# Optimization experiments

Hardware: AMD Instinct MI355X
Metric: run time of the kernel (lower is better)

The kernel has to match this reference:

```python
import jax, jax.numpy as jnp
import numpy as np

B, T, D, H = 4, 2048, 1024, 16
HD = D // H


def setup_inputs() -> dict:
    key = jax.random.key(0)
    ks = jax.random.split(key, 10)
    s = 1.0 / np.sqrt(D)
    # xavier_uniform bound for wbias [T,T]: sqrt(6/(T+T))
    wb_bound = float(np.sqrt(6.0 / (T + T)))
    return {
        "x": jax.random.normal(ks[0], (B, T, D), dtype=jnp.float32),
        "Wq": jax.random.normal(ks[1], (D, D), dtype=jnp.float32) * s,
        "bq": jnp.zeros((D,), dtype=jnp.float32),
        "Wk": jax.random.normal(ks[2], (D, D), dtype=jnp.float32) * s,
        "bk": jnp.zeros((D,), dtype=jnp.float32),
        "Wv": jax.random.normal(ks[3], (D, D), dtype=jnp.float32) * s,
        "bv": jnp.zeros((D,), dtype=jnp.float32),
        "Wo": jax.random.normal(ks[4], (D, D), dtype=jnp.float32) * s,
        "bo": jnp.zeros((D,), dtype=jnp.float32),
        "wbias": jax.random.uniform(ks[5], (T, T), dtype=jnp.float32,
                                    minval=-wb_bound, maxval=wb_bound),
    }


def reference(x, Wq, bq, Wk, bk, Wv, bv, Wo, bo, wbias):
    Bc, Tc, Dc = x.shape
    # projections, split heads: [B, H, T, HD]
    def proj(W, b):
        y = x @ W + b
        return y.reshape(Bc, Tc, H, HD).transpose(0, 2, 1, 3)

    Q = proj(Wq, bq)
    K = proj(Wk, bk)
    V = proj(Wv, bv)

    Q_sig = jax.nn.sigmoid(Q)
    eK = jnp.exp(K)                      # [B,H,T,HD]
    ew = jnp.exp(wbias[:Tc, :Tc])        # [T,T]

    num = jnp.einsum('ts,bhsd->bhtd', ew, eK * V)
    den = jnp.einsum('ts,bhsd->bhtd', ew, eK)
    out = Q_sig * (num / den)            # [B,H,T,HD]

    out = out.transpose(0, 2, 1, 3).reshape(Bc, Tc, Dc)
    return out @ Wo + bo
```

## Files before the change

kernel.cpp:

```cpp
#include <hip/hip_runtime.h>
#include <hip/hip_bf16.h>


#define AS1(p) ((const __attribute__((address_space(1))) void*)(p))
#define AS3(p) ((__attribute__((address_space(3))) void*)(p))

typedef _Float16 half8 __attribute__((ext_vector_type(8)));
typedef _Float16 half4v __attribute__((ext_vector_type(4)));
typedef float floatx16 __attribute__((ext_vector_type(16)));
typedef int intx4 __attribute__((ext_vector_type(4)));
typedef int intx8 __attribute__((ext_vector_type(8)));

__device__ __forceinline__ long frag_off(int r, int k) {
  return (long)(((((r >> 5) * 4 + (k >> 4)) * 2 + ((k >> 3) & 1)) * 32 + (r & 31)) * 8 + (k & 7));
}
__device__ __forceinline__ long off8(int r, int k) {
  return (long)((((((r >> 5) * 2 + ((k >> 6) & 1)) * 2 + ((k >> 4) & 1)) * 2 + ((k >> 5) & 1)) * 32 +
                 (r & 31)) * 16 + (k & 15));
}

__global__ __launch_bounds__(256) void prep_all(
    const float* __restrict__ x, const float* __restrict__ wb, const float* __restrict__ Wq,
    const float* __restrict__ Wk, const float* __restrict__ Wv, const float* __restrict__ Wo,
    _Float16* __restrict__ x_h, char* __restrict__ E8, _Float16* __restrict__ WqkvT,
    _Float16* __restrict__ WoT, float* __restrict__ cs) {
  __shared__ _Float16 lds[64 * 132];
  const int bid = blockIdx.x;
  const int tid = threadIdx.x;

  if (bid >= 1792) {
    float4 z = {0.f, 0.f, 0.f, 0.f};
#pragma unroll
    for (int p = 0; p < 8; ++p) *(float4*)(cs + (p * 256 + tid) * 4) = z;
    return;
  }

  if (bid < 1024) {
    const int tm = bid >> 4, tk = bid & 15;
    const long tbase = (long)bid * 8192;
#pragma unroll
    for (int p = 0; p < 4; ++p) {
      const int s = p * 256 + tid;
      const int r = ((s >> 8) << 5) + (s & 31);
      const int k = ((s >> 6) & 3) * 16 + ((s >> 5) & 1) * 8;
      const float* sp = x + (long)(tm * 128 + r) * 1024 + tk * 64 + k;
      const float4 v0 = *(const float4*)sp;
      const float4 v1 = *(const float4*)(sp + 4);
      half8 h;
      h[0] = (_Float16)v0.x; h[1] = (_Float16)v0.y; h[2] = (_Float16)v0.z; h[3] = (_Float16)v0.w;
      h[4] = (_Float16)v1.x; h[5] = (_Float16)v1.y; h[6] = (_Float16)v1.z; h[7] = (_Float16)v1.w;
      *(half8*)(x_h + tbase + (long)s * 8) = h;
    }
    return;
  }

  if (bid >= 1536) {
    const int e = bid - 1536;
    const int tt = e >> 4, ts = e & 15;
    char* dst = E8 + (long)e * 16384;
#pragma unroll
    for (int p = 0; p < 16; ++p) {
      const int idx = p * 256 + tid;
      const int r = idx >> 5, k = (idx & 31) * 4;
      const float4 v = *(const float4*)(wb + (long)(tt * 128 + r) * 2048 + ts * 128 + k);
      const float e0 = (__expf(v.x) - 1.0f) * 32.0f, e1 = (__expf(v.y) - 1.0f) * 32.0f;
      const float e2 = (__expf(v.z) - 1.0f) * 32.0f, e3 = (__expf(v.w) - 1.0f) * 32.0f;
      int pk = __builtin_amdgcn_cvt_pk_fp8_f32(e0, e1, 0, false);
      pk = __builtin_amdgcn_cvt_pk_fp8_f32(e2, e3, pk, true);
      *(int*)(dst + off8(r, k)) = pk;
    }
    return;
  }

  const int b2 = bid - 1024;
  const float* src0;
  const float* src1 = nullptr;
  _Float16* dst;
  int tn, tk, cb = 0;
  if (b2 < 128) {
    tn = b2 >> 4; tk = b2 & 15; src0 = Wq; dst = WqkvT;
  } else if (b2 < 384) {
    const int t = b2 - 128;
    tn = 8 + (t >> 4); tk = t & 15; cb = (tn - 8) * 64; src0 = Wk; src1 = Wv; dst = WqkvT;
  } else {
    const int t = b2 - 384;
    tn = t >> 4; tk = t & 15; src0 = Wo; dst = WoT;
  }
  if (!src1) {
#pragma unroll
    for (int p = 0; p < 8; ++p) {
      const int kl = p * 8 + (tid >> 5);
      const int cl = (tid & 31) * 4;
      const float4 v = *(const float4*)(src0 + (long)(tk * 64 + kl) * 1024 + tn * 128 + cl);
      half4v h;
      h[0] = (_Float16)v.x; h[1] = (_Float16)v.y; h[2] = (_Float16)v.z; h[3] = (_Float16)v.w;
      *(half4v*)(lds + kl * 132 + cl) = h;
    }
  } else {
#pragma unroll
    for (int m = 0; m < 2; ++m) {
      const float* s = m ? src1 : src0;
      const int rb = m ? 32 : 0;
#pragma unroll
      for (int p = 0; p < 4; ++p) {
        const int kl = p * 16 + (tid >> 4);
        const int cl = (tid & 15) * 4;
        const int rl = (cl >> 5) * 64 + rb + (cl & 31);
        const float4 v = *(const float4*)(s + (long)(tk * 64 + kl) * 1024 + cb + cl);
        half4v h;
        h[0] = (_Float16)v.x; h[1] = (_Float16)v.y; h[2] = (_Float16)v.z; h[3] = (_Float16)v.w;
        *(half4v*)(lds + kl * 132 + rl) = h;
      }
    }
  }
  __syncthreads();
  const long tbase = (long)(tn * 16 + tk) * 8192;
#pragma unroll
  for (int p = 0; p < 4; ++p) {
    const int s = p * 256 + tid;
    const int r = ((s >> 8) << 5) + (s & 31);
    const int kl = ((s >> 6) & 3) * 16 + ((s >> 5) & 1) * 8;
    half8 h;
#pragma unroll
    for (int j = 0; j < 8; ++j) h[j] = lds[(kl + j) * 132 + r];
    *(half8*)(dst + tbase + (long)s * 8) = h;
  }
}

template <int KS>
__device__ __forceinline__ void rd_ab(const _Float16* sA, const _Float16* sB, int wm, int wn,
                                      int lane, half8 (&a)[2], half8 (&b)[2]) {
  a[0] = *(const half8*)(sA + (((wm >> 5) + 0) * 4 + KS) * 512 + lane * 8);
  a[1] = *(const half8*)(sA + (((wm >> 5) + 1) * 4 + KS) * 512 + lane * 8);
  b[0] = *(const half8*)(sB + (((wn >> 5) + 0) * 4 + KS) * 512 + lane * 8);
  b[1] = *(const half8*)(sB + (((wn >> 5) + 1) * 4 + KS) * 512 + lane * 8);
}

__device__ __forceinline__ void mm4(const half8 (&a)[2], const half8 (&b)[2],
                                    floatx16 (&acc)[2][2]) {
  __builtin_amdgcn_s_setprio(1);
#pragma unroll
  for (int mt = 0; mt < 2; ++mt)
#pragma unroll
    for (int nt = 0; nt < 2; ++nt)
      acc[mt][nt] = __builtin_amdgcn_mfma_f32_32x32x16_f16(a[mt], b[nt], acc[mt][nt], 0, 0, 0);
  __builtin_amdgcn_s_setprio(0);
}

template <int VM, bool STAGE, bool LAST>
__device__ __forceinline__ void tile_step(int t, const _Float16* __restrict__ Ablk,
                                          const _Float16* __restrict__ Bblk, _Float16* ring,
                                          int tid, int lane, int wm, int wn,
                                          half8 (&a0)[2], half8 (&b0)[2], half8 (&a1)[2],
                                          half8 (&b1)[2], floatx16 (&acc)[2][2]) {
  const _Float16* sA = ring + (t % 3) * 8192;
  const _Float16* sB = ring + 24576 + (t % 3) * 16384;
  if (STAGE) {
    const int ts = t + 2;
    _Float16* dA = ring + (ts % 3) * 8192 + tid * 8;
    _Float16* dB = ring + 24576 + (ts % 3) * 16384 + tid * 8;
    const _Float16* gA = Ablk + (long)ts * 8192 + tid * 8;
    const _Float16* gB = Bblk + (long)ts * 8192 + tid * 8;
    __builtin_amdgcn_global_load_lds(AS1(gA), AS3(dA), 16, 0, 0);
    __builtin_amdgcn_global_load_lds(AS1(gA + 4096), AS3(dA + 4096), 16, 0, 0);
    __builtin_amdgcn_global_load_lds(AS1(gB), AS3(dB), 16, 0, 0);
    __builtin_amdgcn_global_load_lds(AS1(gB + 4096), AS3(dB + 4096), 16, 0, 0);
    __builtin_amdgcn_global_load_lds(AS1(gB + 131072), AS3(dB + 8192), 16, 0, 0);
    __builtin_amdgcn_global_load_lds(AS1(gB + 131072 + 4096), AS3(dB + 12288), 16, 0, 0);
  }
  rd_ab<1>(sA, sB, wm, wn, lane, a1, b1);
  mm4(a0, b0, acc);
  rd_ab<2>(sA, sB, wm, wn, lane, a0, b0);
  mm4(a1, b1, acc);
  rd_ab<3>(sA, sB, wm, wn, lane, a1, b1);
  mm4(a0, b0, acc);
  if (!LAST) {
    asm volatile("s_waitcnt vmcnt(%0)" ::"i"(VM < 0 ? 0 : VM) : "memory");
    __builtin_amdgcn_s_barrier();
    asm volatile("" ::: "memory");
    const _Float16* nA = ring + ((t + 1) % 3) * 8192;
    const _Float16* nB = ring + 24576 + ((t + 1) % 3) * 16384;
    rd_ab<0>(nA, nB, wm, wn, lane, a0, b0);
  }
  mm4(a1, b1, acc);
}

template <int MODE>
__global__ __launch_bounds__(512, 1) void gemm_bt2(
    const _Float16* __restrict__ A, const _Float16* __restrict__ Bt, void* __restrict__ Cv,
    const float* __restrict__ bias0, const float* __restrict__ bias1,
    const float* __restrict__ bias2, char* __restrict__ Zt8, float* __restrict__ cs) {
  __shared__ __align__(16) _Float16 ring[73728];
  const int tid = threadIdx.x;
  const int wid = tid >> 6, lane = tid & 63;
  const int l32 = lane & 31, khalf = lane >> 5;

  const int f = blockIdx.x;
  const int j = f >> 3;
  const int bxs = (f & 7) * 8 + (j & 7);
  const int bys = j >> 3;
  const int m0 = bxs * 128, n0 = bys * 256;
  const int wm = (wid >> 2) * 64, wn = (wid & 3) * 64;

  const _Float16* Ablk = A + (long)bxs * 131072;
  const _Float16* Bblk = Bt + (long)(bys * 2) * 131072;

#pragma unroll
  for (int t0 = 0; t0 < 2; ++t0) {
    _Float16* dA = ring + t0 * 8192 + tid * 8;
    _Float16* dB = ring + 24576 + t0 * 16384 + tid * 8;
    const _Float16* gA = Ablk + (long)t0 * 8192 + tid * 8;
    const _Float16* gB = Bblk + (long)t0 * 8192 + tid * 8;
    __builtin_amdgcn_global_load_lds(AS1(gA), AS3(dA), 16, 0, 0);
    __builtin_amdgcn_global_load_lds(AS1(gA + 4096), AS3(dA + 4096), 16, 0, 0);
    __builtin_amdgcn_global_load_lds(AS1(gB), AS3(dB), 16, 0, 0);
    __builtin_amdgcn_global_load_lds(AS1(gB + 4096), AS3(dB + 4096), 16, 0, 0);
    __builtin_amdgcn_global_load_lds(AS1(gB + 131072), AS3(dB + 8192), 16, 0, 0);
    __builtin_amdgcn_global_load_lds(AS1(gB + 131072 + 4096), AS3(dB + 12288), 16, 0, 0);
  }
  asm volatile("s_waitcnt vmcnt(6)" ::: "memory");
  __builtin_amdgcn_s_barrier();
  asm volatile("" ::: "memory");

  half8 a0[2], b0[2], a1[2], b1[2];
  rd_ab<0>(ring, ring + 24576, wm, wn, lane, a0, b0);

  floatx16 acc[2][2] = {};
#pragma unroll
  for (int t = 0; t < 14; ++t)
    tile_step<6, true, false>(t, Ablk, Bblk, ring, tid, lane, wm, wn, a0, b0, a1, b1, acc);
  tile_step<0, false, false>(14, Ablk, Bblk, ring, tid, lane, wm, wn, a0, b0, a1, b1, acc);
  tile_step<0, false, true>(15, Ablk, Bblk, ring, tid, lane, wm, wn, a0, b0, a1, b1, acc);

  if (MODE == 0) {
    if (n0 < 1024) {
      _Float16* Qs = (_Float16*)Cv;
#pragma unroll
      for (int mt = 0; mt < 2; ++mt) {
        const long ttile = (m0 + wm + mt * 32) >> 5;
#pragma unroll
        for (int nt = 0; nt < 2; ++nt) {
          const int col = n0 + wn + nt * 32 + l32;
          const float bb = bias0[col];
          const long base = (ttile * 32 + (((n0 + wn) >> 5) + nt)) * 1024;
#pragma unroll
          for (int q = 0; q < 4; ++q) {
            half4v o;
#pragma unroll
            for (int rr = 0; rr < 4; ++rr) {
              const float v = acc[mt][nt][q * 4 + rr] + bb;
              o[rr] = (_Float16)(1.0f / (1.0f + __expf(-v)));
            }
            *(half4v*)(Qs + base + q * 256 + lane * 4) = o;
          }
        }
      }
    } else {
      const int grp = (n0 - 1024 + wn) >> 6;
      const int ch = grp * 32 + l32;
      const float bkc = bias1[ch], bvc = bias2[ch];
      const int jn = grp * 64 + l32;
      const int b = m0 >> 11;
      char* Z8 = Zt8 + (long)b * 4194304 +
                 ((long)(jn >> 7) * 16 + ((m0 & 2047) >> 7)) * 16384;
      const int jnl = jn & 127;
      float sk = 0.f, sz = 0.f;
#pragma unroll
      for (int mt = 0; mt < 2; ++mt) {
#pragma unroll
        for (int q = 0; q < 4; ++q) {
          float ekv[4], ekk[4];
#pragma unroll
          for (int rr = 0; rr < 4; ++rr) {
            const float ek = __expf(acc[mt][0][q * 4 + rr] + bkc);
            const float vv = acc[mt][1][q * 4 + rr] + bvc;
            ekk[rr] = ek;
            ekv[rr] = ek * vv;
            sk += ek;
            sz += ek * vv;
          }
          const int sl = wm + mt * 32 + 4 * khalf + 8 * q;
          int pn = __builtin_amdgcn_cvt_pk_fp8_f32(ekv[0] * 0.25f, ekv[1] * 0.25f, 0, false);
          pn = __builtin_amdgcn_cvt_pk_fp8_f32(ekv[2] * 0.25f, ekv[3] * 0.25f, pn, true);
          int pd = __builtin_amdgcn_cvt_pk_fp8_f32(ekk[0] * 0.25f, ekk[1] * 0.25f, 0, false);
          pd = __builtin_amdgcn_cvt_pk_fp8_f32(ekk[2] * 0.25f, ekk[3] * 0.25f, pd, true);
          *(int*)(Z8 + off8(jnl, sl)) = pn;
          *(int*)(Z8 + off8(jnl + 32, sl)) = pd;
        }
      }
      atomicAdd(&cs[(long)b * 2048 + ch * 2], sz);
      atomicAdd(&cs[(long)b * 2048 + ch * 2 + 1], sk);
    }
    return;
  }

#pragma unroll
  for (int mt = 0; mt < 2; ++mt)
#pragma unroll
    for (int nt = 0; nt < 2; ++nt) {
      const int col = n0 + wn + nt * 32 + l32;
      const float bb = bias0[col];
#pragma unroll
      for (int reg = 0; reg < 16; ++reg) {
        const int row = m0 + wm + mt * 32 + 4 * khalf + 8 * (reg >> 2) + (reg & 3);
        ((float*)Cv)[(long)row * 1024 + col] = acc[mt][nt][reg] + bb;
      }
    }
}

template <int VM, bool STAGE, int SLOT>
__device__ __forceinline__ void g2_phase(int g, char* __restrict__ ringA, char* __restrict__ ringB,
                                         const char* At0, const char* At1,
                                         const char* Bt0, const char* Bt1,
                                         int tid, int lane, int wm, int wn,
                                         floatx16 (&acc)[2][4]) {
  const int l32 = lane & 31, khalf = lane >> 5;
  intx8 a8[2], b8[4];
  {
    const int G = (wm >> 5);
    const char* pa = ringA + SLOT * 16384 + (G >> 2) * 8192 + (G & 3) * 2048 + khalf * 512 + l32 * 16;
    const intx4 alo = *(const intx4*)pa;
    const intx4 ahi = *(const intx4*)(pa + 1024);
    a8[0] = __builtin_shufflevector(alo, ahi, 0, 1, 2, 3, 4, 5, 6, 7);
  }
#pragma unroll
  for (int nt = 0; nt < 2; ++nt) {
    const int Gn = (wn >> 5) + nt;
    const char* pb = ringB + SLOT * 16384 + (Gn >> 2) * 8192 + (Gn & 3) * 2048 + khalf * 512 + l32 * 16;
    const intx4 blo = *(const intx4*)pb;
    const intx4 bhi = *(const intx4*)(pb + 1024);
    b8[nt] = __builtin_shufflevector(blo, bhi, 0, 1, 2, 3, 4, 5, 6, 7);
  }
  {
    const int G = (wm >> 5) + 1;
    const char* pa = ringA + SLOT * 16384 + (G >> 2) * 8192 + (G & 3) * 2048 + khalf * 512 + l32 * 16;
    const intx4 alo = *(const intx4*)pa;
    const intx4 ahi = *(const intx4*)(pa + 1024);
    a8[1] = __builtin_shufflevector(alo, ahi, 0, 1, 2, 3, 4, 5, 6, 7);
  }
#pragma unroll
  for (int nt = 2; nt < 4; ++nt) {
    const int Gn = (wn >> 5) + nt;
    const char* pb = ringB + SLOT * 16384 + (Gn >> 2) * 8192 + (Gn & 3) * 2048 + khalf * 512 + l32 * 16;
    const intx4 blo = *(const intx4*)pb;
    const intx4 bhi = *(const intx4*)(pb + 1024);
    b8[nt] = __builtin_shufflevector(blo, bhi, 0, 1, 2, 3, 4, 5, 6, 7);
  }
  if (STAGE) {
    const int ks = g + 2;
    constexpr int SS = (SLOT + 2) % 3;
    const long gsrc = (long)(ks >> 1) * 16384 + (long)(tid >> 7) * 4096 + (long)(ks & 1) * 2048 +
                      (tid & 127) * 16;
    char* dA = ringA + SS * 16384 + tid * 16;
    char* dB = ringB + SS * 16384 + tid * 16;
    __builtin_amdgcn_global_load_lds(AS1(At0 + gsrc), AS3(dA), 16, 0, 0);
    __builtin_amdgcn_global_load_lds(AS1(At1 + gsrc), AS3(dA + 8192), 16, 0, 0);
    __builtin_amdgcn_global_load_lds(AS1(Bt0 + gsrc), AS3(dB), 16, 0, 0);
    __builtin_amdgcn_global_load_lds(AS1(Bt1 + gsrc), AS3(dB + 8192), 16, 0, 0);
  }
  if constexpr (VM >= 0) {
    asm volatile("s_waitcnt vmcnt(%0)" ::"i"(VM) : "memory");
    __builtin_amdgcn_s_barrier();
  }
  __builtin_amdgcn_s_setprio(1);
#pragma unroll
  for (int nt = 0; nt < 4; ++nt)
#pragma unroll
    for (int mt = 0; mt < 2; ++mt)
      acc[mt][nt] = __builtin_amdgcn_mfma_scale_f32_32x32x64_f8f6f4(
          a8[mt], b8[nt], acc[mt][nt], 0, 0, 0, 127u, 0, 127u);
  __builtin_amdgcn_s_setprio(0);
  if constexpr (VM >= 0) {
    __builtin_amdgcn_s_barrier();
    asm volatile("" ::: "memory");
  }
}

__global__ __launch_bounds__(512, 1) void gemm2_fp8(
    const char* __restrict__ E8, const char* __restrict__ Zt8, _Float16* __restrict__ OH,
    const _Float16* __restrict__ Qsig, const float* __restrict__ cs) {
  __shared__ __align__(16) char ring[98304];
  char* ringA = ring;
  char* ringB = ring + 49152;
  const int tid = threadIdx.x;
  const int wid = tid >> 6, lane = tid & 63;
  const int l32 = lane & 31, khalf = lane >> 5;

  const int f = blockIdx.x;
  const int bxs = f & 7;
  const int bys = (f >> 3) & 7;
  const int bzs = f >> 6;
  const int m0 = bxs * 256;
  const int wm = (wid >> 1) * 64, wn = (wid & 1) * 128;

  const char* At0 = E8 + (long)(bxs * 2) * 262144;
  const char* At1 = At0 + 262144;
  const char* Bt0 = Zt8 + (long)bzs * 4194304 + (long)(bys * 2) * 262144;
  const char* Bt1 = Bt0 + 262144;

#pragma unroll
  for (int ks = 0; ks < 2; ++ks) {
    const long gsrc = (long)(tid >> 7) * 4096 + (long)(ks & 1) * 2048 + (tid & 127) * 16;
    char* dA = ringA + ks * 16384 + tid * 16;
    char* dB = ringB + ks * 16384 + tid * 16;
    __builtin_amdgcn_global_load_lds(AS1(At0 + gsrc), AS3(dA), 16, 0, 0);
    __builtin_amdgcn_global_load_lds(AS1(At1 + gsrc), AS3(dA + 8192), 16, 0, 0);
    __builtin_amdgcn_global_load_lds(AS1(Bt0 + gsrc), AS3(dB), 16, 0, 0);
    __builtin_amdgcn_global_load_lds(AS1(Bt1 + gsrc), AS3(dB + 8192), 16, 0, 0);
  }
  asm volatile("s_waitcnt vmcnt(4)" ::: "memory");
  __builtin_amdgcn_s_barrier();
  asm volatile("" ::: "memory");

  floatx16 acc[2][4] = {};
#pragma unroll 1
  for (int gb = 0; gb < 30; gb += 3) {
    g2_phase<4, true, 0>(gb + 0, ringA, ringB, At0, At1, Bt0, Bt1, tid, lane, wm, wn, acc);
    g2_phase<4, true, 1>(gb + 1, ringA, ringB, At0, At1, Bt0, Bt1, tid, lane, wm, wn, acc);
    g2_phase<4, true, 2>(gb + 2, ringA, ringB, At0, At1, Bt0, Bt1, tid, lane, wm, wn, acc);
  }
  g2_phase<0, false, 0>(30, ringA, ringB, At0, At1, Bt0, Bt1, tid, lane, wm, wn, acc);
  g2_phase<-1, false, 1>(31, ringA, ringB, At0, At1, Bt0, Bt1, tid, lane, wm, wn, acc);

  const int g32b = bys * 4 + (wn >> 6);
#pragma unroll
  for (int mt = 0; mt < 2; ++mt) {
    const long ttile = (long)(bzs * 2048 + m0 + wm + mt * 32) >> 5;
#pragma unroll
    for (int p = 0; p < 2; ++p) {
      const int g32 = g32b + p;
      const int ch = g32 * 32 + l32;
      const float2 c2 = *(const float2*)(cs + (long)bzs * 2048 + ch * 2);
      const long qbase = (ttile * 32 + g32) * 1024;
#pragma unroll
      for (int q = 0; q < 4; ++q) {
        const half4v qv = *(const half4v*)(Qsig + qbase + q * 256 + lane * 4);
#pragma unroll
        for (int rr = 0; rr < 4; ++rr) {
          const int reg = q * 4 + rr;
          const float num = c2.x + acc[mt][2 * p][reg] * 0.125f;
          const float den = c2.y + acc[mt][2 * p + 1][reg] * 0.125f;
          const int r = m0 + wm + mt * 32 + 4 * khalf + 8 * q + rr;
          const int R = bzs * 2048 + r;
          const long off = ((long)(R >> 7) * 16 + (ch >> 6)) * 8192 + frag_off(R & 127, ch & 63);
          OH[off] = (_Float16)((float)qv[rr] * num / den);
        }
      }
    }
  }
}

extern "C" void kernel_launch(void* const* d_in, const int* in_sizes, int n_in, void* d_out,
                              int out_size, void* d_ws, size_t ws_size, hipStream_t stream) {
  const float* x = (const float*)d_in[0];
  const float* Wq = (const float*)d_in[1];
  const float* bq = (const float*)d_in[2];
  const float* Wk = (const float*)d_in[3];
  const float* bk = (const float*)d_in[4];
  const float* Wv = (const float*)d_in[5];
  const float* bv = (const float*)d_in[6];
  const float* Wo = (const float*)d_in[7];
  const float* bo = (const float*)d_in[8];
  const float* wb = (const float*)d_in[9];

  char* ws = (char*)d_ws;
  _Float16* x_h = (_Float16*)(ws + 0);
  _Float16* WqkvT = (_Float16*)(ws + 16777216);
  _Float16* WoT = (_Float16*)(ws + 23068672);
  char* E8 = (char*)(ws + 25165824);
  _Float16* Qsig = (_Float16*)(ws + 29360128);
  char* Zt8 = (char*)(ws + 46137344);
  _Float16* OutHead = (_Float16*)(ws + 62914560);
  float* cs = (float*)(ws + 79691776);

  prep_all<<<1793, 256, 0, stream>>>(x, wb, Wq, Wk, Wv, Wo, x_h, E8, WqkvT, WoT, cs);

  gemm_bt2<0><<<768, 512, 0, stream>>>(x_h, WqkvT, Qsig, bq, bk, bv, Zt8, cs);

  gemm2_fp8<<<256, 512, 0, stream>>>(E8, Zt8, OutHead, Qsig, cs);

  gemm_bt2<2><<<256, 512, 0, stream>>>(OutHead, WoT, d_out, bo, nullptr, nullptr, nullptr, nullptr);
}
```

Baseline: 245.9 us.

## Enlarge GEMM tiles to 256x256 with split-phase A/B staging pipeline

Replaces the 128x256 projection GEMM with a 256x256 tile per block, where each wave computes a 128x64 output using four row fragments. A keeps a three-slot ring, while B keeps a single buffer refilled in K-halves between barriers. Loads are interleaved across four MFMA phases per K-step. This raises arithmetic intensity and halves the block count. The cost is more barriers per step, more accumulator registers, and fewer blocks (384 and 128), which may underfill the 256 CUs.

```diff
diff --git a/kernel.cpp b/kernel.cpp
--- a/kernel.cpp
+++ b/kernel.cpp
@@ -10,6 +10,10 @@
 typedef float floatx16 __attribute__((ext_vector_type(16)));
 typedef int intx4 __attribute__((ext_vector_type(4)));
 typedef int intx8 __attribute__((ext_vector_type(8)));
+
+__device__ __forceinline__ floatx16 MM(half8 a, half8 b, floatx16 c) {
+  return __builtin_amdgcn_mfma_f32_32x32x16_f16(a, b, c, 0, 0, 0);
+}
 
 __device__ __forceinline__ long frag_off(int r, int k) {
   return (long)(((((r >> 5) * 4 + (k >> 4)) * 2 + ((k >> 3) & 1)) * 32 + (r & 31)) * 8 + (k & 7));
@@ -127,128 +131,182 @@
   }
 }
 
-template <int KS>
-__device__ __forceinline__ void rd_ab(const _Float16* sA, const _Float16* sB, int wm, int wn,
-                                      int lane, half8 (&a)[2], half8 (&b)[2]) {
-  a[0] = *(const half8*)(sA + (((wm >> 5) + 0) * 4 + KS) * 512 + lane * 8);
-  a[1] = *(const half8*)(sA + (((wm >> 5) + 1) * 4 + KS) * 512 + lane * 8);
-  b[0] = *(const half8*)(sB + (((wn >> 5) + 0) * 4 + KS) * 512 + lane * 8);
-  b[1] = *(const half8*)(sB + (((wn >> 5) + 1) * 4 + KS) * 512 + lane * 8);
-}
-
-__device__ __forceinline__ void mm4(const half8 (&a)[2], const half8 (&b)[2],
-                                    floatx16 (&acc)[2][2]) {
+template <bool SA, bool SB, int VM2>
+__device__ __forceinline__ void step3(
+    int t, const _Float16* __restrict__ As0, const _Float16* __restrict__ As1,
+    const _Float16* __restrict__ Bb, _Float16* ldsA, _Float16* ldsB,
+    int tid, int lane, int wmh, const _Float16* bb, floatx16 (&acc)[4][2]) {
+  const _Float16* sA = ldsA + (t % 3) * 16384 + wmh * 8192 + lane * 8;
+  half8 a[4], b[4];
+
+  asm volatile("s_waitcnt vmcnt(2)" ::: "memory");
+  __builtin_amdgcn_s_barrier();
+  asm volatile("" ::: "memory");
+  a[0] = *(const half8*)(sA + 0 * 512);
+  a[1] = *(const half8*)(sA + 1 * 512);
+  a[2] = *(const half8*)(sA + 4 * 512);
+  a[3] = *(const half8*)(sA + 5 * 512);
+  b[0] = *(const half8*)(bb + 0);
+  b[1] = *(const half8*)(bb + 512);
+  b[2] = *(const half8*)(bb + 1024);
+  b[3] = *(const half8*)(bb + 1536);
+  if (SA) {
+    _Float16* d = ldsA + ((t + 2) % 3) * 16384 + tid * 8;
+    const _Float16* g = As0 + (long)(t + 2) * 8192 + tid * 8;
+    __builtin_amdgcn_global_load_lds(AS1(g), AS3(d), 16, 0, 0);
+    __builtin_amdgcn_global_load_lds(AS1(g + 4096), AS3(d + 4096), 16, 0, 0);
+  }
   __builtin_amdgcn_s_setprio(1);
-#pragma unroll
-  for (int mt = 0; mt < 2; ++mt)
-#pragma unroll
-    for (int nt = 0; nt < 2; ++nt)
-      acc[mt][nt] = __builtin_amdgcn_mfma_f32_32x32x16_f16(a[mt], b[nt], acc[mt][nt], 0, 0, 0);
+  acc[0][0] = MM(a[0], b[0], acc[0][0]); acc[0][0] = MM(a[1], b[1], acc[0][0]);
+  acc[0][1] = MM(a[0], b[2], acc[0][1]); acc[0][1] = MM(a[1], b[3], acc[0][1]);
+  acc[1][0] = MM(a[2], b[0], acc[1][0]); acc[1][0] = MM(a[3], b[1], acc[1][0]);
+  acc[1][1] = MM(a[2], b[2], acc[1][1]); acc[1][1] = MM(a[3], b[3], acc[1][1]);
   __builtin_amdgcn_s_setprio(0);
-}
-
-template <int VM, bool STAGE, bool LAST>
-__device__ __forceinline__ void tile_step(int t, const _Float16* __restrict__ Ablk,
-                                          const _Float16* __restrict__ Bblk, _Float16* ring,
-                                          int tid, int lane, int wm, int wn,
-                                          half8 (&a0)[2], half8 (&b0)[2], half8 (&a1)[2],
-                                          half8 (&b1)[2], floatx16 (&acc)[2][2]) {
-  const _Float16* sA = ring + (t % 3) * 8192;
-  const _Float16* sB = ring + 24576 + (t % 3) * 16384;
-  if (STAGE) {
-    const int ts = t + 2;
-    _Float16* dA = ring + (ts % 3) * 8192 + tid * 8;
-    _Float16* dB = ring + 24576 + (ts % 3) * 16384 + tid * 8;
-    const _Float16* gA = Ablk + (long)ts * 8192 + tid * 8;
-    const _Float16* gB = Bblk + (long)ts * 8192 + tid * 8;
-    __builtin_amdgcn_global_load_lds(AS1(gA), AS3(dA), 16, 0, 0);
-    __builtin_amdgcn_global_load_lds(AS1(gA + 4096), AS3(dA + 4096), 16, 0, 0);
-    __builtin_amdgcn_global_load_lds(AS1(gB), AS3(dB), 16, 0, 0);
-    __builtin_amdgcn_global_load_lds(AS1(gB + 4096), AS3(dB + 4096), 16, 0, 0);
-    __builtin_amdgcn_global_load_lds(AS1(gB + 131072), AS3(dB + 8192), 16, 0, 0);
-    __builtin_amdgcn_global_load_lds(AS1(gB + 131072 + 4096), AS3(dB + 12288), 16, 0, 0);
-  }
-  rd_ab<1>(sA, sB, wm, wn, lane, a1, b1);
-  mm4(a0, b0, acc);
-  rd_ab<2>(sA, sB, wm, wn, lane, a0, b0);
-  mm4(a1, b1, acc);
-  rd_ab<3>(sA, sB, wm, wn, lane, a1, b1);
-  mm4(a0, b0, acc);
-  if (!LAST) {
-    asm volatile("s_waitcnt vmcnt(%0)" ::"i"(VM < 0 ? 0 : VM) : "memory");
-    __builtin_amdgcn_s_barrier();
-    asm volatile("" ::: "memory");
-    const _Float16* nA = ring + ((t + 1) % 3) * 8192;
-    const _Float16* nB = ring + 24576 + ((t + 1) % 3) * 16384;
-    rd_ab<0>(nA, nB, wm, wn, lane, a0, b0);
-  }
-  mm4(a1, b1, acc);
+  __builtin_amdgcn_s_barrier();
+  asm volatile("" ::: "memory");
+
+  a[0] = *(const half8*)(sA + 8 * 512);
+  a[1] = *(const half8*)(sA + 9 * 512);
+  a[2] = *(const half8*)(sA + 12 * 512);
+  a[3] = *(const half8*)(sA + 13 * 512);
+  if (SA) {
+    _Float16* d = ldsA + ((t + 2) % 3) * 16384 + 8192 + tid * 8;
+    const _Float16* g = As1 + (long)(t + 2) * 8192 + tid * 8;
+    __builtin_amdgcn_global_load_lds(AS1(g), AS3(d), 16, 0, 0);
+    __builtin_amdgcn_global_load_lds(AS1(g + 4096), AS3(d + 4096), 16, 0, 0);
+  }
+  __builtin_amdgcn_s_setprio(1);
+  acc[2][0] = MM(a[0], b[0], acc[2][0]); acc[2][0] = MM(a[1], b[1], acc[2][0]);
+  acc[2][1] = MM(a[0], b[2], acc[2][1]); acc[2][1] = MM(a[1], b[3], acc[2][1]);
+  acc[3][0] = MM(a[2], b[0], acc[3][0]); acc[3][0] = MM(a[3], b[1], acc[3][0]);
+  acc[3][1] = MM(a[2], b[2], acc[3][1]); acc[3][1] = MM(a[3], b[3], acc[3][1]);
+  __builtin_amdgcn_s_setprio(0);
+  __builtin_amdgcn_s_barrier();
+  asm volatile("" ::: "memory");
+
+  asm volatile("s_waitcnt vmcnt(%0)" ::"i"(VM2) : "memory");
+  __builtin_amdgcn_s_barrier();
+  asm volatile("" ::: "memory");
+  a[0] = *(const half8*)(sA + 2 * 512);
+  a[1] = *(const half8*)(sA + 3 * 512);
+  a[2] = *(const half8*)(sA + 6 * 512);
+  a[3] = *(const half8*)(sA + 7 * 512);
+  b[0] = *(const half8*)(bb + 8192 + 0);
+  b[1] = *(const half8*)(bb + 8192 + 512);
+  b[2] = *(const half8*)(bb + 8192 + 1024);
+  b[3] = *(const half8*)(bb + 8192 + 1536);
+  if (SB) {
+#pragma unroll
+    for (int c = 0; c < 2; ++c) {
+      const int L = tid * 8 + c * 4096;
+      const _Float16* g = Bb + (long)(L >> 12) * 131072 + (long)(t + 1) * 8192 +
+                          ((L >> 10) & 3) * 2048 + (L & 1023);
+      __builtin_amdgcn_global_load_lds(AS1(g), AS3(ldsB + L), 16, 0, 0);
+    }
+  }
+  __builtin_amdgcn_s_setprio(1);
+  acc[0][0] = MM(a[0], b[0], acc[0][0]); acc[0][0] = MM(a[1], b[1], acc[0][0]);
+  acc[0][1] = MM(a[0], b[2], acc[0][1]); acc[0][1] = MM(a[1], b[3], acc[0][1]);
+  acc[1][0] = MM(a[2], b[0], acc[1][0]); acc[1][0] = MM(a[3], b[1], acc[1][0]);
+  acc[1][1] = MM(a[2], b[2], acc[1][1]); acc[1][1] = MM(a[3], b[3], acc[1][1]);
+  __builtin_amdgcn_s_setprio(0);
+  __builtin_amdgcn_s_barrier();
+  asm volatile("" ::: "memory");
+
+  a[0] = *(const half8*)(sA + 10 * 512);
+  a[1] = *(const half8*)(sA + 11 * 512);
+  a[2] = *(const half8*)(sA + 14 * 512);
+  a[3] = *(const half8*)(sA + 15 * 512);
+  if (SB) {
+#pragma unroll
+    for (int c = 0; c < 2; ++c) {
+      const int L = tid * 8 + c * 4096;
+      const _Float16* g = Bb + (long)(L >> 12) * 131072 + (long)(t + 1) * 8192 +
+                          ((L >> 10) & 3) * 2048 + 1024 + (L & 1023);
+      __builtin_amdgcn_global_load_lds(AS1(g), AS3(ldsB + 8192 + L), 16, 0, 0);
+    }
+  }
+  __builtin_amdgcn_s_setprio(1);
+  acc[2][0] = MM(a[0], b[0], acc[2][0]); acc[2][0] = MM(a[1], b[1], acc[2][0]);
+  acc[2][1] = MM(a[0], b[2], acc[2][1]); acc[2][1] = MM(a[1], b[3], acc[2][1]);
+  acc[3][0] = MM(a[2], b[0], acc[3][0]); acc[3][0] = MM(a[3], b[1], acc[3][0]);
+  acc[3][1] = MM(a[2], b[2], acc[3][1]); acc[3][1] = MM(a[3], b[3], acc[3][1]);
+  __builtin_amdgcn_s_setprio(0);
+  __builtin_amdgcn_s_barrier();
+  asm volatile("" ::: "memory");
 }
 
 template <int MODE>
-__global__ __launch_bounds__(512, 1) void gemm_bt2(
+__global__ __launch_bounds__(512, 1) void gemm_bt3(
     const _Float16* __restrict__ A, const _Float16* __restrict__ Bt, void* __restrict__ Cv,
     const float* __restrict__ bias0, const float* __restrict__ bias1,
     const float* __restrict__ bias2, char* __restrict__ Zt8, float* __restrict__ cs) {
-  __shared__ __align__(16) _Float16 ring[73728];
+  __shared__ __align__(16) _Float16 ring[65536];
+  _Float16* ldsA = ring;
+  _Float16* ldsB = ring + 49152;
   const int tid = threadIdx.x;
   const int wid = tid >> 6, lane = tid & 63;
   const int l32 = lane & 31, khalf = lane >> 5;
 
   const int f = blockIdx.x;
-  const int j = f >> 3;
-  const int bxs = (f & 7) * 8 + (j & 7);
-  const int bys = j >> 3;
-  const int m0 = bxs * 128, n0 = bys * 256;
-  const int wm = (wid >> 2) * 64, wn = (wid & 3) * 64;
-
-  const _Float16* Ablk = A + (long)bxs * 131072;
-  const _Float16* Bblk = Bt + (long)(bys * 2) * 131072;
-
-#pragma unroll
-  for (int t0 = 0; t0 < 2; ++t0) {
-    _Float16* dA = ring + t0 * 8192 + tid * 8;
-    _Float16* dB = ring + 24576 + t0 * 16384 + tid * 8;
-    const _Float16* gA = Ablk + (long)t0 * 8192 + tid * 8;
-    const _Float16* gB = Bblk + (long)t0 * 8192 + tid * 8;
-    __builtin_amdgcn_global_load_lds(AS1(gA), AS3(dA), 16, 0, 0);
-    __builtin_amdgcn_global_load_lds(AS1(gA + 4096), AS3(dA + 4096), 16, 0, 0);
-    __builtin_amdgcn_global_load_lds(AS1(gB), AS3(dB), 16, 0, 0);
-    __builtin_amdgcn_global_load_lds(AS1(gB + 4096), AS3(dB + 4096), 16, 0, 0);
-    __builtin_amdgcn_global_load_lds(AS1(gB + 131072), AS3(dB + 8192), 16, 0, 0);
-    __builtin_amdgcn_global_load_lds(AS1(gB + 131072 + 4096), AS3(dB + 12288), 16, 0, 0);
-  }
-  asm volatile("s_waitcnt vmcnt(6)" ::: "memory");
-  __builtin_amdgcn_s_barrier();
-  asm volatile("" ::: "memory");
-
-  half8 a0[2], b0[2], a1[2], b1[2];
-  rd_ab<0>(ring, ring + 24576, wm, wn, lane, a0, b0);
-
-  floatx16 acc[2][2] = {};
+  const int bxs = (f & 7) * 4 + ((f >> 3) & 3);
+  const int bys = f >> 5;
+  const int m0 = bxs * 256, n0 = bys * 256;
+  const int wmh = wid >> 2;
+  const int wm = wmh * 128;
+  const int wn = (wid & 3) * 64;
+
+  const _Float16* As0 = A + (long)(bxs * 2) * 131072;
+  const _Float16* As1 = As0 + 131072;
+  const _Float16* Bb = Bt + (long)(bys * 2) * 131072;
+
+  const _Float16* bb = ldsB + ((wn >> 7) * 4 + ((wn & 127) >> 5)) * 1024 + lane * 8;
+
+#pragma unroll
+  for (int tt = 0; tt < 2; ++tt) {
+#pragma unroll
+    for (int ph = 0; ph < 2; ++ph) {
+      const _Float16* g = (ph ? As1 : As0) + (long)tt * 8192 + tid * 8;
+      _Float16* d = ldsA + tt * 16384 + ph * 8192 + tid * 8;
+      __builtin_amdgcn_global_load_lds(AS1(g), AS3(d), 16, 0, 0);
+      __builtin_amdgcn_global_load_lds(AS1(g + 4096), AS3(d + 4096), 16, 0, 0);
+    }
+  }
+#pragma unroll
+  for (int ksh = 0; ksh < 2; ++ksh) {
+#pragma unroll
+    for (int c = 0; c < 2; ++c) {
+      const int L = tid * 8 + c * 4096;
+      const _Float16* g = Bb + (long)(L >> 12) * 131072 + ((L >> 10) & 3) * 2048 +
+                          ksh * 1024 + (L & 1023);
+      __builtin_amdgcn_global_load_lds(AS1(g), AS3(ldsB + ksh * 8192 + L), 16, 0, 0);
+    }
+  }
+
+  floatx16 acc[4][2] = {};
 #pragma unroll
   for (int t = 0; t < 14; ++t)
-    tile_step<6, true, false>(t, Ablk, Bblk, ring, tid, lane, wm, wn, a0, b0, a1, b1, acc);
-  tile_step<0, false, false>(14, Ablk, Bblk, ring, tid, lane, wm, wn, a0, b0, a1, b1, acc);
-  tile_step<0, false, true>(15, Ablk, Bblk, ring, tid, lane, wm, wn, a0, b0, a1, b1, acc);
+    step3<true, true, 4>(t, As0, As1, Bb, ldsA, ldsB, tid, lane, wmh, bb, acc);
+  step3<false, true, 0>(14, As0, As1, Bb, ldsA, ldsB, tid, lane, wmh, bb, acc);
+  step3<false, false, 0>(15, As0, As1, Bb, ldsA, ldsB, tid, lane, wmh, bb, acc);
 
   if (MODE == 0) {
     if (n0 < 1024) {
       _Float16* Qs = (_Float16*)Cv;
 #pragma unroll
-      for (int mt = 0; mt < 2; ++mt) {
+      for (int mt = 0; mt < 4; ++mt) {
         const long ttile = (m0 + wm + mt * 32) >> 5;
 #pragma unroll
         for (int nt = 0; nt < 2; ++nt) {
           const int col = n0 + wn + nt * 32 + l32;
-          const float bb = bias0[col];
-          const long base = (ttile * 32 + (((n0 + wn) >> 5) + nt)) * 1024;
+          const float bb0 = bias0[col];
+          const long base = (ttile * 32 + ((n0 + wn) >> 5) + nt) * 1024;
 #pragma unroll
           for (int q = 0; q < 4; ++q) {
             half4v o;
 #pragma unroll
             for (int rr = 0; rr < 4; ++rr) {
-              const float v = acc[mt][nt][q * 4 + rr] + bb;
+              const float v = acc[mt][nt][q * 4 + rr] + bb0;
               o[rr] = (_Float16)(1.0f / (1.0f + __expf(-v)));
             }
             *(half4v*)(Qs + base + q * 256 + lane * 4) = o;
@@ -261,12 +319,12 @@
       const float bkc = bias1[ch], bvc = bias2[ch];
       const int jn = grp * 64 + l32;
       const int b = m0 >> 11;
-      char* Z8 = Zt8 + (long)b * 4194304 +
-                 ((long)(jn >> 7) * 16 + ((m0 & 2047) >> 7)) * 16384;
+      const int tc = ((m0 + wm) & 2047) >> 7;
+      char* Z8 = Zt8 + (long)b * 4194304 + ((long)(jn >> 7) * 16 + tc) * 16384;
       const int jnl = jn & 127;
       float sk = 0.f, sz = 0.f;
 #pragma unroll
-      for (int mt = 0; mt < 2; ++mt) {
+      for (int mt = 0; mt < 4; ++mt) {
 #pragma unroll
         for (int q = 0; q < 4; ++q) {
           float ekv[4], ekk[4];
@@ -279,7 +337,7 @@
             sk += ek;
             sz += ek * vv;
           }
-          const int sl = wm + mt * 32 + 4 * khalf + 8 * q;
+          const int sl = mt * 32 + 4 * khalf + 8 * q;
           int pn = __builtin_amdgcn_cvt_pk_fp8_f32(ekv[0] * 0.25f, ekv[1] * 0.25f, 0, false);
           pn = __builtin_amdgcn_cvt_pk_fp8_f32(ekv[2] * 0.25f, ekv[3] * 0.25f, pn, true);
           int pd = __builtin_amdgcn_cvt_pk_fp8_f32(ekk[0] * 0.25f, ekk[1] * 0.25f, 0, false);
@@ -295,15 +353,15 @@
   }
 
 #pragma unroll
-  for (int mt = 0; mt < 2; ++mt)
+  for (int mt = 0; mt < 4; ++mt)
 #pragma unroll
     for (int nt = 0; nt < 2; ++nt) {
       const int col = n0 + wn + nt * 32 + l32;
-      const float bb = bias0[col];
+      const float bb0 = bias0[col];
 #pragma unroll
       for (int reg = 0; reg < 16; ++reg) {
         const int row = m0 + wm + mt * 32 + 4 * khalf + 8 * (reg >> 2) + (reg & 3);
-        ((float*)Cv)[(long)row * 1024 + col] = acc[mt][nt][reg] + bb;
+        ((float*)Cv)[(long)row * 1024 + col] = acc[mt][nt][reg] + bb0;
       }
     }
 }
@@ -475,9 +533,9 @@
 
   prep_all<<<1793, 256, 0, stream>>>(x, wb, Wq, Wk, Wv, Wo, x_h, E8, WqkvT, WoT, cs);
 
-  gemm_bt2<0><<<768, 512, 0, stream>>>(x_h, WqkvT, Qsig, bq, bk, bv, Zt8, cs);
+  gemm_bt3<0><<<384, 512, 0, stream>>>(x_h, WqkvT, Qsig, bq, bk, bv, Zt8, cs);
 
   gemm2_fp8<<<256, 512, 0, stream>>>(E8, Zt8, OutHead, Qsig, cs);
 
-  gemm_bt2<2><<<256, 512, 0, stream>>>(OutHead, WoT, d_out, bo, nullptr, nullptr, nullptr, nullptr);
-}
+  gemm_bt3<2><<<128, 512, 0, stream>>>(OutHead, WoT, d_out, bo, nullptr, nullptr, nullptr, nullptr);
+}
```

After: 247.4 us. No clear change (+0.6%).
